# Kernel optimization log

Hardware: AMD Instinct MI355X
Metric: run time of the kernel (lower is better)

The kernel has to match this reference:

```python
import jax, jax.numpy as jnp
import numpy as np

B, N, C = 2, 2048, 1024
H = 16
D = C // H  # head_dim = 64
SCALE = D ** -0.5


def setup_inputs() -> dict:
    key = jax.random.key(0)
    ks = jax.random.split(key, 9)
    s = C ** -0.5  # ~ torch Linear default init scale
    return {
        "x": jax.random.normal(ks[0], (B, N, C), dtype=jnp.float32),
        "Wq": jax.random.uniform(ks[1], (C, C), jnp.float32, -s, s),
        "bq": jax.random.uniform(ks[2], (C,), jnp.float32, -s, s),
        "Wk": jax.random.uniform(ks[3], (C, C), jnp.float32, -s, s),
        "bk": jax.random.uniform(ks[4], (C,), jnp.float32, -s, s),
        "Wv": jax.random.uniform(ks[5], (C, C), jnp.float32, -s, s),
        "bv": jax.random.uniform(ks[6], (C,), jnp.float32, -s, s),
        "Wo": jax.random.uniform(ks[7], (C, C), jnp.float32, -s, s),
        "bo": jax.random.uniform(ks[8], (C,), jnp.float32, -s, s),
    }


def reference(x, Wq, bq, Wk, bk, Wv, bv, Wo, bo):
    # Projections: [B,N,C] -> [B,H,N,D]
    def split_heads(t):
        return t.reshape(B, N, H, D).transpose(0, 2, 1, 3)

    q = split_heads(x @ Wq.T + bq)
    k = split_heads(x @ Wk.T + bk)
    v = split_heads(x @ Wv.T + bv)

    scores = jnp.einsum("bhnd,bhmd->bhnm", q, k) * SCALE  # [B,H,N,N]
    attn = jax.nn.softmax(scores, axis=-1)
    out = jnp.einsum("bhnm,bhmd->bhnd", attn, v)  # [B,H,N,D]
    out = out.transpose(0, 2, 1, 3).reshape(B, N, C)
    return out @ Wo.T + bo
```

## Files before the change

### kernel.cpp

```cpp
#include <hip/hip_runtime.h>
#include <stdint.h>


typedef _Float16 h8 __attribute__((ext_vector_type(8)));
typedef _Float16 h4 __attribute__((ext_vector_type(4)));
typedef float f4 __attribute__((ext_vector_type(4)));
typedef float f16f __attribute__((ext_vector_type(16)));
typedef uint32_t u32;
typedef u32 u32x4 __attribute__((ext_vector_type(4)));

#define AS1(p) ((const __attribute__((address_space(1))) void*)(p))
#define AS3(p) ((__attribute__((address_space(3))) void*)(p))

template <int ITERS>
__device__ __forceinline__ void stage128B(const _Float16* g, int ldk, _Float16* s, int tid) {
#pragma unroll
  for (int j = 0; j < ITERS; ++j) {
    int off = j * 4096 + tid * 16;
    int row = off >> 7;
    int ch = (off >> 4) & 7;
    int gch = ch ^ (row & 7);
    __builtin_amdgcn_global_load_lds(AS1(g + row * ldk + gch * 8), AS3(s + (off >> 1)), 16, 0, 0);
  }
}

__device__ __forceinline__ void stage8k_v(const _Float16* g, _Float16* s, int tid) {
  int off = tid * 16;
  int row = off >> 7;
  int ch = (off >> 4) & 7;
  int gch = ch ^ (row & 7);
  __builtin_amdgcn_global_load_lds(AS1(g + row * 2048 + gch * 8), AS3(s + (off >> 1)), 16, 0, 0);
}
__device__ __forceinline__ void stage8k_k(const _Float16* g, _Float16* s, int tid) {
  int off = tid * 16;
  int row = off >> 7;
  int ch = (off >> 4) & 7;
  int gch = ch ^ ((row & 3) | ((row >> 1) & 4));
  __builtin_amdgcn_global_load_lds(AS1(g + row * 64 + gch * 8), AS3(s + (off >> 1)), 16, 0, 0);
}

__device__ __forceinline__ h8 frag64(const _Float16* s, int row, int g) {
  return *(const h8*)(s + row * 64 + ((g ^ (row & 7)) << 3));
}

__global__ void cvt_all(const float* __restrict__ x, const float* __restrict__ Wq,
                        const float* __restrict__ Wk, const float* __restrict__ Wv,
                        const float* __restrict__ Wo, _Float16* __restrict__ xh,
                        _Float16* __restrict__ q, _Float16* __restrict__ k,
                        _Float16* __restrict__ v, _Float16* __restrict__ o) {
  int blk = blockIdx.x;
  const float* src; _Float16* dst; int off;
  if (blk < 4096)      { src = x;  dst = xh; off = blk; }
  else if (blk < 5120) { src = Wq; dst = q;  off = blk - 4096; }
  else if (blk < 6144) { src = Wk; dst = k;  off = blk - 5120; }
  else if (blk < 7168) { src = Wv; dst = v;  off = blk - 6144; }
  else                 { src = Wo; dst = o;  off = blk - 7168; }
  int i = off * 1024 + threadIdx.x * 4;
  f4 vv = *(const f4*)(src + i);
  h4 ov;
  ov[0] = (_Float16)vv[0]; ov[1] = (_Float16)vv[1]; ov[2] = (_Float16)vv[2]; ov[3] = (_Float16)vv[3];
  *(h4*)(dst + i) = ov;
}

__global__ __launch_bounds__(256, 3) void gemm_qkv(
    const _Float16* __restrict__ X,
    const _Float16* __restrict__ W0, const _Float16* __restrict__ W1, const _Float16* __restrict__ W2,
    const float* __restrict__ b0, const float* __restrict__ b1, const float* __restrict__ b2,
    _Float16* __restrict__ O0, _Float16* __restrict__ O1, _Float16* __restrict__ O2) {
  __shared__ _Float16 As[128 * 64];
  __shared__ _Float16 Bs[128 * 64];
  int z = blockIdx.z;
  const _Float16* W = (z == 0) ? W0 : (z == 1) ? W1 : W2;
  const float* bias = (z == 0) ? b0 : (z == 1) ? b1 : b2;

  int tid = threadIdx.x;
  int lane = tid & 63, wave = tid >> 6;
  int quad = lane >> 4, l15 = lane & 15;
  int wm = (wave >> 1) << 6, wn = (wave & 1) << 6;
  int m0 = blockIdx.y << 7, n0 = blockIdx.x << 7;

  f4 acc[4][4] = {};
  for (int k0 = 0; k0 < 1024; k0 += 64) {
    stage128B<4>(X + m0 * 1024 + k0, 1024, As, tid);
    stage128B<4>(W + n0 * 1024 + k0, 1024, Bs, tid);
    __syncthreads();
#pragma unroll
    for (int ks = 0; ks < 2; ++ks) {
      h8 af[4], bf[4];
#pragma unroll
      for (int i = 0; i < 4; ++i) af[i] = frag64(As, wm + i * 16 + l15, ks * 4 + quad);
#pragma unroll
      for (int i = 0; i < 4; ++i) bf[i] = frag64(Bs, wn + i * 16 + l15, ks * 4 + quad);
#pragma unroll
      for (int mi = 0; mi < 4; ++mi)
#pragma unroll
        for (int ni = 0; ni < 4; ++ni)
          acc[mi][ni] = __builtin_amdgcn_mfma_f32_16x16x32_f16(af[mi], bf[ni], acc[mi][ni], 0, 0, 0);
    }
    __syncthreads();
  }

  if (z == 2) {
#pragma unroll
    for (int mi = 0; mi < 4; ++mi) {
#pragma unroll
      for (int ni = 0; ni < 4; ++ni) {
        int o = n0 + wn + ni * 16 + l15;
        float bv = bias[o];
        int h = o >> 6, dd = o & 63;
        int m = m0 + wm + mi * 16 + quad * 4;
        int b = m >> 11, n = m & 2047;
        h4 v;
#pragma unroll
        for (int r = 0; r < 4; ++r) v[r] = (_Float16)(acc[mi][ni][r] + bv);
        *(h4*)(O2 + (((b * 16 + h) * 64 + dd) * 2048 + n)) = v;
      }
    }
  } else {
    float scale = (z == 0) ? 0.125f * 1.44269504089f : 1.0f;
    _Float16* Out = (z == 0) ? O0 : O1;
#pragma unroll
    for (int mi = 0; mi < 4; ++mi) {
#pragma unroll
      for (int ni = 0; ni < 4; ++ni) {
        int o = n0 + wn + ni * 16 + l15;
        float bv = bias[o];
        int h = o >> 6, d = o & 63;
#pragma unroll
        for (int r = 0; r < 4; ++r) {
          int m = m0 + wm + mi * 16 + quad * 4 + r;
          int b = m >> 11, n = m & 2047;
          float v = (acc[mi][ni][r] + bv) * scale;
          Out[(((b * 16 + h) * 2048 + n) << 6) + d] = (_Float16)v;
        }
      }
    }
  }
}

__global__ __launch_bounds__(256, 3) void gemm_out(
    const _Float16* __restrict__ A, const _Float16* __restrict__ W,
    const float* __restrict__ bias, float* __restrict__ Out) {
  __shared__ _Float16 As[128 * 64];
  __shared__ _Float16 Bs[64 * 64];
  int tid = threadIdx.x;
  int lane = tid & 63, wave = tid >> 6;
  int quad = lane >> 4, l15 = lane & 15;
  int wm = (wave >> 1) << 6, wn = (wave & 1) << 5;
  int m0 = blockIdx.y << 7, n0 = blockIdx.x << 6;

  f4 acc[4][2] = {};
  for (int k0 = 0; k0 < 1024; k0 += 64) {
    stage128B<4>(A + m0 * 1024 + k0, 1024, As, tid);
    stage128B<2>(W + n0 * 1024 + k0, 1024, Bs, tid);
    __syncthreads();
#pragma unroll
    for (int ks = 0; ks < 2; ++ks) {
      h8 af[4], bf[2];
#pragma unroll
      for (int i = 0; i < 4; ++i) af[i] = frag64(As, wm + i * 16 + l15, ks * 4 + quad);
#pragma unroll
      for (int i = 0; i < 2; ++i) bf[i] = frag64(Bs, wn + i * 16 + l15, ks * 4 + quad);
#pragma unroll
      for (int mi = 0; mi < 4; ++mi)
#pragma unroll
        for (int ni = 0; ni < 2; ++ni)
          acc[mi][ni] = __builtin_amdgcn_mfma_f32_16x16x32_f16(af[mi], bf[ni], acc[mi][ni], 0, 0, 0);
    }
    __syncthreads();
  }
#pragma unroll
  for (int mi = 0; mi < 4; ++mi) {
#pragma unroll
    for (int ni = 0; ni < 2; ++ni) {
      int o = n0 + wn + ni * 16 + l15;
      float bv = bias[o];
#pragma unroll
      for (int r = 0; r < 4; ++r) {
        int m = m0 + wm + mi * 16 + quad * 4 + r;
        Out[m * 1024 + o] = acc[mi][ni][r] + bv;
      }
    }
  }
}

__global__ __launch_bounds__(512, 4) void attn(
    const _Float16* __restrict__ Q, const _Float16* __restrict__ Kv,
    const _Float16* __restrict__ Vt, _Float16* __restrict__ AO) {
  __shared__ _Float16 smem[6 * 4096];
  _Float16* Ksb = smem;
  _Float16* Vsb = smem + 3 * 4096;

  int tid = threadIdx.x, lane = tid & 63, wave = tid >> 6;
  int h = lane >> 5, l31 = lane & 31;
  int p = wave & 1, qg = wave >> 1;
  int bh = blockIdx.y, q0 = blockIdx.x << 7;

  const _Float16* Qb = Q + (bh * 2048 + q0 + qg * 32 + l31) * 64;
  h8 qf[4];
#pragma unroll
  for (int ks4 = 0; ks4 < 4; ++ks4)
    qf[ks4] = *(const h8*)(Qb + ks4 * 16 + h * 8);

  int krow = (l31 & 19) | ((l31 & 4) << 1) | ((l31 & 8) >> 1);
  int kbase = (p * 32 + krow) * 64;
  int kx = (krow & 3) | ((krow >> 1) & 4);
  int vx = l31 & 7;

  const _Float16* Kb = Kv + bh * 131072;
  const _Float16* Vb = Vt + bh * 131072;
  f16f oacc[2] = {};
  float lsum = 0.f;

  stage8k_k(Kb, Ksb, tid);
  stage8k_v(Vb, Vsb, tid);
  stage8k_k(Kb + 4096, Ksb + 4096, tid);
  stage8k_v(Vb + 64, Vsb + 4096, tid);

  int bp = 0;
  for (int ph = 0; ph < 32; ++ph) {
    if (ph < 31) {
      asm volatile("s_waitcnt vmcnt(2)\n\ts_barrier" ::: "memory");
    } else {
      asm volatile("s_waitcnt vmcnt(0)\n\ts_barrier" ::: "memory");
    }
    const _Float16* Kst = Ksb + bp * 4096;
    const _Float16* Vst = Vsb + bp * 4096;

    f16f sacc = {};
#pragma unroll
    for (int ks4 = 0; ks4 < 4; ++ks4) {
      h8 kf = *(const h8*)(Kst + kbase + (((ks4 * 2 + h) ^ kx) << 3));
      sacc = __builtin_amdgcn_mfma_f32_32x32x16_f16(kf, qf[ks4], sacc, 0, 0, 0);
    }

    u32 pkw[8];
#pragma unroll
    for (int i = 0; i < 8; ++i) {
      float pa = __builtin_amdgcn_exp2f(sacc[2 * i]);
      float pb = __builtin_amdgcn_exp2f(sacc[2 * i + 1]);
      lsum += pa + pb;
      pkw[i] = __builtin_bit_cast(u32, __builtin_amdgcn_cvt_pkrtz(pa, pb));
    }

#pragma unroll
    for (int s = 0; s < 2; ++s) {
      u32x4 pw = {pkw[4 * s], pkw[4 * s + 1], pkw[4 * s + 2], pkw[4 * s + 3]};
      h8 pb = __builtin_bit_cast(h8, pw);
      int ch = (((p << 2) | (s << 1) | h) ^ vx) << 3;
#pragma unroll
      for (int dt = 0; dt < 2; ++dt) {
        h8 vf = *(const h8*)(Vst + (dt * 32 + l31) * 64 + ch);
        oacc[dt] = __builtin_amdgcn_mfma_f32_32x32x16_f16(vf, pb, oacc[dt], 0, 0, 0);
      }
    }

    if (ph < 30) {
      int sl = bp ? bp - 1 : 2;
      stage8k_k(Kb + (ph + 2) * 4096, Ksb + sl * 4096, tid);
      stage8k_v(Vb + (ph + 2) * 64, Vsb + sl * 4096, tid);
    }
    bp = (bp == 2) ? 0 : bp + 1;
  }

  __syncthreads();
  float* cb = (float*)smem;
  if (p) {
    float* w = cb + (qg * 64 + lane) * 33;
#pragma unroll
    for (int i = 0; i < 16; ++i) w[i] = oacc[0][i];
#pragma unroll
    for (int i = 0; i < 16; ++i) w[16 + i] = oacc[1][i];
    w[32] = lsum;
  }
  __syncthreads();
  if (!p) {
    const float* r = cb + (qg * 64 + lane) * 33;
#pragma unroll
    for (int i = 0; i < 16; ++i) oacc[0][i] += r[i];
#pragma unroll
    for (int i = 0; i < 16; ++i) oacc[1][i] += r[16 + i];
    lsum += r[32];

    float l = lsum + __shfl_xor(lsum, 32);
    float inv = 1.0f / l;
    int b = bh >> 4, hh = bh & 15;
    int n = q0 + qg * 32 + l31;
    _Float16* base = AO + (b * 2048 + n) * 1024 + hh * 64;
#pragma unroll
    for (int dt = 0; dt < 2; ++dt) {
#pragma unroll
      for (int b2 = 0; b2 < 4; ++b2) {
        h4 o;
#pragma unroll
        for (int a = 0; a < 4; ++a) o[a] = (_Float16)(oacc[dt][b2 * 4 + a] * inv);
        *(h4*)(base + dt * 32 + b2 * 8 + h * 4) = o;
      }
    }
  }
}

extern "C" void kernel_launch(void* const* d_in, const int* in_sizes, int n_in,
                              void* d_out, int out_size, void* d_ws, size_t ws_size,
                              hipStream_t stream) {
  const float* x = (const float*)d_in[0];
  const float* Wq = (const float*)d_in[1];
  const float* bq = (const float*)d_in[2];
  const float* Wk = (const float*)d_in[3];
  const float* bk = (const float*)d_in[4];
  const float* Wv = (const float*)d_in[5];
  const float* bv = (const float*)d_in[6];
  const float* Wo = (const float*)d_in[7];
  const float* bo = (const float*)d_in[8];
  float* out = (float*)d_out;

  char* w = (char*)d_ws;
  _Float16* xh  = (_Float16*)(w);
  _Float16* Wqh = (_Float16*)(w + (8u << 20));
  _Float16* Wkh = (_Float16*)(w + (10u << 20));
  _Float16* Wvh = (_Float16*)(w + (12u << 20));
  _Float16* Woh = (_Float16*)(w + (14u << 20));
  _Float16* Qh  = (_Float16*)(w + (16u << 20));
  _Float16* Kh  = (_Float16*)(w + (24u << 20));
  _Float16* Vth = (_Float16*)(w + (32u << 20));
  _Float16* AOh = xh;

  cvt_all<<<8192, 256, 0, stream>>>(x, Wq, Wk, Wv, Wo, xh, Wqh, Wkh, Wvh, Woh);
  gemm_qkv<<<dim3(8, 32, 3), 256, 0, stream>>>(xh, Wqh, Wkh, Wvh, bq, bk, bv, Qh, Kh, Vth);
  attn<<<dim3(16, 32), 512, 0, stream>>>(Qh, Kh, Vth, AOh);
  gemm_out<<<dim3(16, 32), 256, 0, stream>>>(AOh, Woh, bo, out);
}
```

Baseline: 181.8 us.

## Process two query sub-tiles per wave in attention, halving block threads

The attention block goes from 512 to 256 threads, and each wave now handles 64 query rows as two 32-row sub-tiles that share every K and V fragment read from LDS. Each thread issues two async staging loads per tile instead of one, and the wait count is adjusted to match. This halves LDS fragment reads per MFMA and the number of waves contending at barriers. The cost is double the accumulator registers per thread and less thread-level parallelism per block, with launch bounds lowered to (256,2).

```diff
diff --git a/kernel.cpp b/kernel.cpp
--- a/kernel.cpp
+++ b/kernel.cpp
@@ -24,19 +24,25 @@
   }
 }
 
-__device__ __forceinline__ void stage8k_v(const _Float16* g, _Float16* s, int tid) {
-  int off = tid * 16;
-  int row = off >> 7;
-  int ch = (off >> 4) & 7;
-  int gch = ch ^ (row & 7);
-  __builtin_amdgcn_global_load_lds(AS1(g + row * 2048 + gch * 8), AS3(s + (off >> 1)), 16, 0, 0);
-}
-__device__ __forceinline__ void stage8k_k(const _Float16* g, _Float16* s, int tid) {
-  int off = tid * 16;
-  int row = off >> 7;
-  int ch = (off >> 4) & 7;
-  int gch = ch ^ ((row & 3) | ((row >> 1) & 4));
-  __builtin_amdgcn_global_load_lds(AS1(g + row * 64 + gch * 8), AS3(s + (off >> 1)), 16, 0, 0);
+__device__ __forceinline__ void stage_v(const _Float16* g, _Float16* s, int tid) {
+#pragma unroll
+  for (int j = 0; j < 2; ++j) {
+    int off = j * 4096 + tid * 16;
+    int row = off >> 7;
+    int ch = (off >> 4) & 7;
+    int gch = ch ^ (row & 7);
+    __builtin_amdgcn_global_load_lds(AS1(g + row * 2048 + gch * 8), AS3(s + (off >> 1)), 16, 0, 0);
+  }
+}
+__device__ __forceinline__ void stage_k(const _Float16* g, _Float16* s, int tid) {
+#pragma unroll
+  for (int j = 0; j < 2; ++j) {
+    int off = j * 4096 + tid * 16;
+    int row = off >> 7;
+    int ch = (off >> 4) & 7;
+    int gch = ch ^ ((row & 3) | ((row >> 1) & 4));
+    __builtin_amdgcn_global_load_lds(AS1(g + row * 64 + gch * 8), AS3(s + (off >> 1)), 16, 0, 0);
+  }
 }
 
 __device__ __forceinline__ h8 frag64(const _Float16* s, int row, int g) {
@@ -184,7 +190,7 @@
   }
 }
 
-__global__ __launch_bounds__(512, 4) void attn(
+__global__ __launch_bounds__(256, 2) void attn(
     const _Float16* __restrict__ Q, const _Float16* __restrict__ Kv,
     const _Float16* __restrict__ Vt, _Float16* __restrict__ AO) {
   __shared__ _Float16 smem[6 * 4096];
@@ -196,11 +202,13 @@
   int p = wave & 1, qg = wave >> 1;
   int bh = blockIdx.y, q0 = blockIdx.x << 7;
 
-  const _Float16* Qb = Q + (bh * 2048 + q0 + qg * 32 + l31) * 64;
-  h8 qf[4];
-#pragma unroll
-  for (int ks4 = 0; ks4 < 4; ++ks4)
-    qf[ks4] = *(const h8*)(Qb + ks4 * 16 + h * 8);
+  const _Float16* Qb = Q + (bh * 2048 + q0 + qg * 64 + l31) * 64;
+  h8 qf[2][4];
+#pragma unroll
+  for (int qs = 0; qs < 2; ++qs)
+#pragma unroll
+    for (int ks4 = 0; ks4 < 4; ++ks4)
+      qf[qs][ks4] = *(const h8*)(Qb + qs * 32 * 64 + ks4 * 16 + h * 8);
 
   int krow = (l31 & 19) | ((l31 & 4) << 1) | ((l31 & 8) >> 1);
   int kbase = (p * 32 + krow) * 64;
@@ -209,56 +217,63 @@
 
   const _Float16* Kb = Kv + bh * 131072;
   const _Float16* Vb = Vt + bh * 131072;
-  f16f oacc[2] = {};
-  float lsum = 0.f;
-
-  stage8k_k(Kb, Ksb, tid);
-  stage8k_v(Vb, Vsb, tid);
-  stage8k_k(Kb + 4096, Ksb + 4096, tid);
-  stage8k_v(Vb + 64, Vsb + 4096, tid);
+  f16f oacc[2][2] = {};
+  float lsum[2] = {0.f, 0.f};
+
+  stage_k(Kb, Ksb, tid);
+  stage_v(Vb, Vsb, tid);
+  stage_k(Kb + 4096, Ksb + 4096, tid);
+  stage_v(Vb + 64, Vsb + 4096, tid);
 
   int bp = 0;
   for (int ph = 0; ph < 32; ++ph) {
     if (ph < 31) {
-      asm volatile("s_waitcnt vmcnt(2)\n\ts_barrier" ::: "memory");
+      asm volatile("s_waitcnt vmcnt(4)\n\ts_barrier" ::: "memory");
     } else {
       asm volatile("s_waitcnt vmcnt(0)\n\ts_barrier" ::: "memory");
     }
     const _Float16* Kst = Ksb + bp * 4096;
     const _Float16* Vst = Vsb + bp * 4096;
 
-    f16f sacc = {};
+    f16f sacc[2] = {};
 #pragma unroll
     for (int ks4 = 0; ks4 < 4; ++ks4) {
       h8 kf = *(const h8*)(Kst + kbase + (((ks4 * 2 + h) ^ kx) << 3));
-      sacc = __builtin_amdgcn_mfma_f32_32x32x16_f16(kf, qf[ks4], sacc, 0, 0, 0);
-    }
-
-    u32 pkw[8];
-#pragma unroll
-    for (int i = 0; i < 8; ++i) {
-      float pa = __builtin_amdgcn_exp2f(sacc[2 * i]);
-      float pb = __builtin_amdgcn_exp2f(sacc[2 * i + 1]);
-      lsum += pa + pb;
-      pkw[i] = __builtin_bit_cast(u32, __builtin_amdgcn_cvt_pkrtz(pa, pb));
+      sacc[0] = __builtin_amdgcn_mfma_f32_32x32x16_f16(kf, qf[0][ks4], sacc[0], 0, 0, 0);
+      sacc[1] = __builtin_amdgcn_mfma_f32_32x32x16_f16(kf, qf[1][ks4], sacc[1], 0, 0, 0);
+    }
+
+    u32 pkw[2][8];
+#pragma unroll
+    for (int qs = 0; qs < 2; ++qs) {
+#pragma unroll
+      for (int i = 0; i < 8; ++i) {
+        float pa = __builtin_amdgcn_exp2f(sacc[qs][2 * i]);
+        float pb = __builtin_amdgcn_exp2f(sacc[qs][2 * i + 1]);
+        lsum[qs] += pa + pb;
+        pkw[qs][i] = __builtin_bit_cast(u32, __builtin_amdgcn_cvt_pkrtz(pa, pb));
+      }
     }
 
 #pragma unroll
     for (int s = 0; s < 2; ++s) {
-      u32x4 pw = {pkw[4 * s], pkw[4 * s + 1], pkw[4 * s + 2], pkw[4 * s + 3]};
-      h8 pb = __builtin_bit_cast(h8, pw);
+      u32x4 pw0 = {pkw[0][4 * s], pkw[0][4 * s + 1], pkw[0][4 * s + 2], pkw[0][4 * s + 3]};
+      u32x4 pw1 = {pkw[1][4 * s], pkw[1][4 * s + 1], pkw[1][4 * s + 2], pkw[1][4 * s + 3]};
+      h8 pb0 = __builtin_bit_cast(h8, pw0);
+      h8 pb1 = __builtin_bit_cast(h8, pw1);
       int ch = (((p << 2) | (s << 1) | h) ^ vx) << 3;
 #pragma unroll
       for (int dt = 0; dt < 2; ++dt) {
         h8 vf = *(const h8*)(Vst + (dt * 32 + l31) * 64 + ch);
-        oacc[dt] = __builtin_amdgcn_mfma_f32_32x32x16_f16(vf, pb, oacc[dt], 0, 0, 0);
+        oacc[0][dt] = __builtin_amdgcn_mfma_f32_32x32x16_f16(vf, pb0, oacc[0][dt], 0, 0, 0);
+        oacc[1][dt] = __builtin_amdgcn_mfma_f32_32x32x16_f16(vf, pb1, oacc[1][dt], 0, 0, 0);
       }
     }
 
     if (ph < 30) {
       int sl = bp ? bp - 1 : 2;
-      stage8k_k(Kb + (ph + 2) * 4096, Ksb + sl * 4096, tid);
-      stage8k_v(Vb + (ph + 2) * 64, Vsb + sl * 4096, tid);
+      stage_k(Kb + (ph + 2) * 4096, Ksb + sl * 4096, tid);
+      stage_v(Vb + (ph + 2) * 64, Vsb + sl * 4096, tid);
     }
     bp = (bp == 2) ? 0 : bp + 1;
   }
@@ -266,35 +281,44 @@
   __syncthreads();
   float* cb = (float*)smem;
   if (p) {
-    float* w = cb + (qg * 64 + lane) * 33;
-#pragma unroll
-    for (int i = 0; i < 16; ++i) w[i] = oacc[0][i];
-#pragma unroll
-    for (int i = 0; i < 16; ++i) w[16 + i] = oacc[1][i];
-    w[32] = lsum;
+    float* w = cb + (qg * 64 + lane) * 66;
+#pragma unroll
+    for (int qs = 0; qs < 2; ++qs)
+#pragma unroll
+      for (int dt = 0; dt < 2; ++dt)
+#pragma unroll
+        for (int i = 0; i < 16; ++i) w[(qs * 2 + dt) * 16 + i] = oacc[qs][dt][i];
+    w[64] = lsum[0];
+    w[65] = lsum[1];
   }
   __syncthreads();
   if (!p) {
-    const float* r = cb + (qg * 64 + lane) * 33;
-#pragma unroll
-    for (int i = 0; i < 16; ++i) oacc[0][i] += r[i];
-#pragma unroll
-    for (int i = 0; i < 16; ++i) oacc[1][i] += r[16 + i];
-    lsum += r[32];
-
-    float l = lsum + __shfl_xor(lsum, 32);
-    float inv = 1.0f / l;
+    const float* r = cb + (qg * 64 + lane) * 66;
+#pragma unroll
+    for (int qs = 0; qs < 2; ++qs)
+#pragma unroll
+      for (int dt = 0; dt < 2; ++dt)
+#pragma unroll
+        for (int i = 0; i < 16; ++i) oacc[qs][dt][i] += r[(qs * 2 + dt) * 16 + i];
+    lsum[0] += r[64];
+    lsum[1] += r[65];
+
     int b = bh >> 4, hh = bh & 15;
-    int n = q0 + qg * 32 + l31;
-    _Float16* base = AO + (b * 2048 + n) * 1024 + hh * 64;
-#pragma unroll
-    for (int dt = 0; dt < 2; ++dt) {
-#pragma unroll
-      for (int b2 = 0; b2 < 4; ++b2) {
-        h4 o;
-#pragma unroll
-        for (int a = 0; a < 4; ++a) o[a] = (_Float16)(oacc[dt][b2 * 4 + a] * inv);
-        *(h4*)(base + dt * 32 + b2 * 8 + h * 4) = o;
+#pragma unroll
+    for (int qs = 0; qs < 2; ++qs) {
+      float l = lsum[qs] + __shfl_xor(lsum[qs], 32);
+      float inv = 1.0f / l;
+      int n = q0 + qg * 64 + qs * 32 + l31;
+      _Float16* base = AO + (b * 2048 + n) * 1024 + hh * 64;
+#pragma unroll
+      for (int dt = 0; dt < 2; ++dt) {
+#pragma unroll
+        for (int b2 = 0; b2 < 4; ++b2) {
+          h4 o;
+#pragma unroll
+          for (int a = 0; a < 4; ++a) o[a] = (_Float16)(oacc[qs][dt][b2 * 4 + a] * inv);
+          *(h4*)(base + dt * 32 + b2 * 8 + h * 4) = o;
+        }
       }
     }
   }
@@ -327,6 +351,6 @@
 
   cvt_all<<<8192, 256, 0, stream>>>(x, Wq, Wk, Wv, Wo, xh, Wqh, Wkh, Wvh, Woh);
   gemm_qkv<<<dim3(8, 32, 3), 256, 0, stream>>>(xh, Wqh, Wkh, Wvh, bq, bk, bv, Qh, Kh, Vth);
-  attn<<<dim3(16, 32), 512, 0, stream>>>(Qh, Kh, Vth, AOh);
+  attn<<<dim3(16, 32), 256, 0, stream>>>(Qh, Kh, Vth, AOh);
   gemm_out<<<dim3(16, 32), 256, 0, stream>>>(AOh, Woh, bo, out);
 }
```

Measured after the change: 179.8 us. No clear change (-1.1%).
